# Kernel tuning notes

Hardware: AMD Instinct MI355X
Metric: run time of the kernel (lower is better)

The kernel has to match this reference:

```python
import jax, jax.numpy as jnp
import numpy as np

D_MODEL = 1024
D_STATE = 16
D_CONV = 4
EXPAND = 2
D_INNER = EXPAND * D_MODEL  # 2048
DT_RANK = 64  # ceil(1024/16)
BATCH = 2
SEQ = 1024
EPS = 1e-5


def _causal_depthwise_conv(x, w, b):
    # x: (B, L, D); w: (D, K) depthwise kernel; b: (D,)
    K = w.shape[1]
    xp = jnp.pad(x, ((0, 0), (K - 1, 0), (0, 0)))            # left-pad for causality
    out = jax.lax.conv_general_dilated(
        xp.transpose(0, 2, 1),          # (B, D, L+K-1)
        w[:, None, :],                  # (D, 1, K)
        window_strides=(1,), padding='VALID',
        feature_group_count=w.shape[0])
    return out.transpose(0, 2, 1) + b   # (B, L, D)


def _ssm_dir(xs, conv_w, conv_b, xproj_w, dt_w, dt_b, A_log, D_skip):
    # xs: (B, L, D_INNER)
    Bsz = xs.shape[0]
    xc = jax.nn.silu(_causal_depthwise_conv(xs, conv_w, conv_b))
    x_dbl = xc @ xproj_w                                        # (B, L, dt_rank + 2N)
    dt, B_ssm, C_ssm = jnp.split(x_dbl, [DT_RANK, DT_RANK + D_STATE], axis=-1)
    dt = jax.nn.softplus(dt @ dt_w + dt_b)                      # (B, L, D_INNER)
    A = -jnp.exp(A_log)                                         # (D_INNER, N)
    dA = jnp.exp(dt[..., None] * A)                             # (B, L, D_INNER, N)
    dBu = dt[..., None] * B_ssm[:, :, None, :] * xc[..., None]  # (B, L, D_INNER, N)

    def step(h, inp):
        dAt, dBut, ct = inp          # (B,D,N), (B,D,N), (B,N)
        h = dAt * h + dBut
        y = jnp.einsum('bdn,bn->bd', h, ct)
        return h, y

    h0 = jnp.zeros((Bsz, D_INNER, D_STATE), dtype=xs.dtype)
    _, ys = jax.lax.scan(step, h0,
                         (jnp.moveaxis(dA, 1, 0), jnp.moveaxis(dBu, 1, 0), jnp.moveaxis(C_ssm, 1, 0)))
    y = jnp.moveaxis(ys, 0, 1)                                  # (B, L, D_INNER)
    return y + xc * D_skip


def _layernorm(x, gamma, beta):
    mu = jnp.mean(x, axis=-1, keepdims=True)
    var = jnp.mean(jnp.square(x - mu), axis=-1, keepdims=True)
    return (x - mu) * jax.lax.rsqrt(var + EPS) * gamma + beta


def setup_inputs() -> dict:
    key = jax.random.key(0)
    ks = jax.random.split(key, 24)
    s = 0.02
    A_init = jnp.log(jnp.tile(jnp.arange(1, D_STATE + 1, dtype=jnp.float32)[None, :], (D_INNER, 1)))
    # dt bias init (inverse-softplus of small dt), as in the torch module
    dt0 = jnp.exp(jax.random.uniform(ks[20], (D_INNER,)) * (np.log(0.1) - np.log(0.001)) + np.log(0.001))
    dt0 = jnp.clip(dt0, 1e-4)
    inv_dt = dt0 + jnp.log(-jnp.expm1(-dt0))
    return {
        'x': jax.random.normal(ks[0], (BATCH, SEQ, D_MODEL), jnp.float32),
        'gamma': jnp.ones((D_MODEL,), jnp.float32),
        'beta': jnp.zeros((D_MODEL,), jnp.float32),
        'in_w': jax.random.normal(ks[1], (D_MODEL, 2 * D_INNER), jnp.float32) * s,
        'conv_w': jax.random.normal(ks[2], (D_INNER, D_CONV), jnp.float32) * s,
        'conv_b': jnp.zeros((D_INNER,), jnp.float32),
        'xproj_w': jax.random.normal(ks[3], (D_INNER, DT_RANK + 2 * D_STATE), jnp.float32) * s,
        'dt_w': jax.random.normal(ks[4], (DT_RANK, D_INNER), jnp.float32) * s,
        'dt_b': inv_dt,
        'A_log': A_init,
        'D_skip': jnp.ones((D_INNER,), jnp.float32),
        'conv_w_b': jax.random.normal(ks[5], (D_INNER, D_CONV), jnp.float32) * s,
        'conv_b_b': jnp.zeros((D_INNER,), jnp.float32),
        'xproj_w_b': jax.random.normal(ks[6], (D_INNER, DT_RANK + 2 * D_STATE), jnp.float32) * s,
        'dt_w_b': jax.random.normal(ks[7], (DT_RANK, D_INNER), jnp.float32) * s,
        'dt_b_b': inv_dt,
        'A_log_b': A_init,
        'D_skip_b': jnp.ones((D_INNER,), jnp.float32),
        'merge_w': jax.random.normal(ks[8], (2 * D_INNER, D_INNER), jnp.float32) * s,
        'out_w': jax.random.normal(ks[9], (D_INNER, D_MODEL), jnp.float32) * s,
    }


def reference(x, gamma, beta, in_w, conv_w, conv_b, xproj_w, dt_w, dt_b, A_log, D_skip,
              conv_w_b, conv_b_b, xproj_w_b, dt_w_b, dt_b_b, A_log_b, D_skip_b,
              merge_w, out_w):
    residual = x
    h = _layernorm(x, gamma, beta)
    xz = h @ in_w                               # (B, L, 2*D_INNER)
    xs, z = jnp.split(xz, 2, axis=-1)
    y_fwd = _ssm_dir(xs, conv_w, conv_b, xproj_w, dt_w, dt_b, A_log, D_skip)
    y_back = _ssm_dir(xs[:, ::-1], conv_w_b, conv_b_b, xproj_w_b, dt_w_b, dt_b_b, A_log_b, D_skip_b)[:, ::-1]
    y = jnp.concatenate([y_fwd, y_back], axis=-1) @ merge_w
    y = y * jax.nn.silu(z)
    y = y @ out_w
    return residual + y
```

## Files before the change

### kernel.cpp

```cpp
#include <hip/hip_runtime.h>
#include <hip/hip_bf16.h>
#include <math.h>

typedef __hip_bfloat16 bf16;
typedef unsigned int u32;
typedef __attribute__((ext_vector_type(8))) short bf16x8;
typedef __attribute__((ext_vector_type(4))) float f32x4;

#define BATCH 2
#define SEQ 1024
#define DM 1024
#define DI 2048
#define NST 16
#define DTR 64
#define XDN 96
#define XDP_LD 128
#define T_TOK 2048
#define N2 4096
#define NCHUNK 32
#define CLEN 32

static __device__ __forceinline__ float b2f(bf16 v) { return __bfloat162float(v); }
static __device__ __forceinline__ float bits2f(unsigned short u) {
    return __uint_as_float(((unsigned)u) << 16);
}

static __device__ __forceinline__ void gload_lds16(const void* g, void* l) {
    __builtin_amdgcn_global_load_lds((__attribute__((address_space(1))) u32*)(size_t)g,
                                     (__attribute__((address_space(3))) u32*)l, 16, 0, 0);
}

#define SBAR() do { asm volatile("" ::: "memory"); __builtin_amdgcn_s_barrier(); asm volatile("" ::: "memory"); } while (0)

static __device__ void tileT(const float* __restrict__ in, bf16* __restrict__ out,
                             int K, int N, int t, float (*tb)[33]) {
    int nt = N >> 5;
    int bx = (t % nt) << 5, by = (t / nt) << 5;
    int tx = threadIdx.x & 31, r0 = threadIdx.x >> 5;
#pragma unroll
    for (int r = r0; r < 32; r += 8)
        tb[r][tx] = in[(size_t)(by + r) * N + bx + tx];
    __syncthreads();
#pragma unroll
    for (int r = r0; r < 32; r += 8)
        out[(size_t)(bx + r) * K + by + tx] = __float2bfloat16(tb[tx][r]);
}

#define LN_BLKS   T_TOK
#define INW_T     ((N2 / 32) * (DM / 32))
#define OUTW_T    ((DM / 32) * (DI / 32))
#define MRGW_T    ((DI / 32) * (N2 / 32))
#define SMALL_BLK ((2 * XDP_LD * DI + 2 * DI * DTR) / 256)

__global__ __launch_bounds__(256) void prep_mega(const float* __restrict__ x,
                                                 const float* __restrict__ gamma,
                                                 const float* __restrict__ beta,
                                                 bf16* __restrict__ H,
                                                 const float* __restrict__ in_w, bf16* __restrict__ in_wT,
                                                 const float* __restrict__ out_w, bf16* __restrict__ out_wT,
                                                 const float* __restrict__ merge_w, bf16* __restrict__ merge_wT,
                                                 const float* __restrict__ xpf, const float* __restrict__ xpb,
                                                 bf16* __restrict__ XPF, bf16* __restrict__ XPB,
                                                 const float* __restrict__ dtwf, const float* __restrict__ dtwb,
                                                 bf16* __restrict__ dtwT) {
    __shared__ float tbuf[32][33];
    __shared__ float red[8];
    int bid = blockIdx.x;
    int tid = threadIdx.x;

    if (bid < LN_BLKS) {
        int t = bid;
        float xv[4];
        float s = 0.f, s2 = 0.f;
#pragma unroll
        for (int k = 0; k < 4; ++k) {
            float v = x[(size_t)t * DM + k * 256 + tid];
            xv[k] = v; s += v; s2 += v * v;
        }
#pragma unroll
        for (int off = 32; off; off >>= 1) {
            s  += __shfl_down(s, off);
            s2 += __shfl_down(s2, off);
        }
        int wid = tid >> 6, lane = tid & 63;
        if (!lane) { red[wid] = s; red[4 + wid] = s2; }
        __syncthreads();
        if (tid == 0) {
            float S = red[0] + red[1] + red[2] + red[3];
            float S2 = red[4] + red[5] + red[6] + red[7];
            float mu = S * (1.f / DM);
            float var = S2 * (1.f / DM) - mu * mu;
            red[0] = mu;
            red[1] = rsqrtf(var + 1e-5f);
        }
        __syncthreads();
        float mu = red[0], rs = red[1];
#pragma unroll
        for (int k = 0; k < 4; ++k) {
            int i = k * 256 + tid;
            H[(size_t)t * DM + i] = __float2bfloat16((xv[k] - mu) * rs * gamma[i] + beta[i]);
        }
        return;
    }
    bid -= LN_BLKS;
    if (bid < INW_T)  { tileT(in_w, in_wT, DM, N2, bid, tbuf); return; }
    bid -= INW_T;
    if (bid < OUTW_T) { tileT(out_w, out_wT, DI, DM, bid, tbuf); return; }
    bid -= OUTW_T;
    if (bid < MRGW_T) { tileT(merge_w, merge_wT, N2, DI, bid, tbuf); return; }
    bid -= MRGW_T;
    int idx = bid * 256 + tid;
    if (idx < 2 * XDP_LD * DI) {
        int dir = idx >= XDP_LD * DI;
        int i = idx - dir * (XDP_LD * DI);
        int n = i >> 11;
        int k = i & (DI - 1);
        float v = (n < XDN) ? (dir ? xpb : xpf)[k * XDN + n] : 0.f;
        (dir ? XPB : XPF)[i] = __float2bfloat16(v);
    } else {
        int j = idx - 2 * XDP_LD * DI;
        int dir = j >= DI * DTR;
        int e = j - dir * (DI * DTR);
        int n = e >> 6;
        int k = e & 63;
        dtwT[(size_t)dir * DI * DTR + n * DTR + k] =
            __float2bfloat16((dir ? dtwb : dtwf)[(size_t)k * DI + n]);
    }
}

template <int EPI>
__global__ __launch_bounds__(256) void mfma_gemm(const bf16* __restrict__ A,
                                                 const bf16* __restrict__ BT,
                                                 const bf16* __restrict__ BT2, int bysplit,
                                                 bf16* __restrict__ Cb,
                                                 const float* __restrict__ resid,
                                                 float* __restrict__ outf,
                                                 bf16* __restrict__ Pb,
                                                 const float* __restrict__ bias1,
                                                 const float* __restrict__ bias2,
                                                 int M, int N, int K) {
    __shared__ bf16 As[8192];
    __shared__ bf16 Bs[8192];
    int tid = threadIdx.x;
    int wave = tid >> 6, lane = tid & 63;
    int q = lane >> 4, ln16 = lane & 15;
    int bm = blockIdx.y * 128, bn = blockIdx.x * 128;
    int wm = (wave >> 1) * 64, wn = (wave & 1) * 64;
    const bf16* Bt = ((int)blockIdx.y < bysplit) ? BT : BT2;

    int ks = K / gridDim.z;
    int kb = blockIdx.z * ks;

    f32x4 zf; zf[0] = zf[1] = zf[2] = zf[3] = 0.f;
    f32x4 acc[4][4];
#pragma unroll
    for (int i = 0; i < 4; ++i)
#pragma unroll
        for (int j = 0; j < 4; ++j) acc[i][j] = zf;

    for (int k0 = kb; k0 < kb + ks; k0 += 64) {
#pragma unroll
        for (int i = 0; i < 4; ++i) {
            int s = wave * 256 + i * 64 + lane;
            int kg = s >> 7, m = s & 127;
            gload_lds16(&A[(size_t)(bm + m) * K + k0 + kg * 8], &As[(wave * 256 + i * 64) * 8]);
            gload_lds16(&Bt[(size_t)(bn + m) * K + k0 + kg * 8], &Bs[(wave * 256 + i * 64) * 8]);
        }
        __syncthreads();
#pragma unroll
        for (int kk = 0; kk < 2; ++kk) {
            bf16x8 af[4], bfr[4];
#pragma unroll
            for (int i = 0; i < 4; ++i) {
                af[i]  = *(const bf16x8*)&As[(((kk * 4 + q) * 128) + (wm + i * 16 + ln16)) * 8];
                bfr[i] = *(const bf16x8*)&Bs[(((kk * 4 + q) * 128) + (wn + i * 16 + ln16)) * 8];
            }
#pragma unroll
            for (int i = 0; i < 4; ++i)
#pragma unroll
                for (int j = 0; j < 4; ++j)
                    acc[i][j] = __builtin_amdgcn_mfma_f32_16x16x32_bf16(af[i], bfr[j], acc[i][j], 0, 0, 0);
        }
        __syncthreads();
    }

    size_t pbase = (size_t)blockIdx.z * M * N;
#pragma unroll
    for (int i = 0; i < 4; ++i)
#pragma unroll
        for (int r = 0; r < 4; ++r) {
            int row = bm + wm + i * 16 + q * 4 + r;
            const float* bias = (EPI == 4) ? ((row < T_TOK) ? bias1 : bias2) : nullptr;
#pragma unroll
            for (int j = 0; j < 4; ++j) {
                int col = bn + wn + j * 16 + ln16;
                size_t idx = (size_t)row * N + col;
                float v = acc[i][j][r];
                if (EPI == 0)      Cb[idx] = __float2bfloat16(v);
                else if (EPI == 1) outf[idx] = resid[idx] + v;
                else if (EPI == 2) outf[idx] = v;
                else if (EPI == 3) Pb[pbase + idx] = __float2bfloat16(v);
                else {
                    float t = v + bias[col];
                    float sp = (t > 20.f) ? t : log1pf(__expf(t));
                    Cb[idx] = __float2bfloat16(sp);
                }
            }
        }
}

template <int EPI>
__global__ __launch_bounds__(512, 2) void gemm256(const bf16* __restrict__ A,
                                                  const bf16* __restrict__ BT,
                                                  bf16* __restrict__ Cb,
                                                  bf16* __restrict__ Pb,
                                                  int M, int N, int K) {
    __shared__ bf16 LA[4][8192];
    __shared__ bf16 LB[4][8192];
    int tid = threadIdx.x;
    int wave = tid >> 6, lane = tid & 63;
    int q = lane >> 4, ln16 = lane & 15;
    int bm = blockIdx.y * 256, bn = blockIdx.x * 256;
    int wm = (wave >> 2) * 128, wn = (wave & 3) * 64;
    int ksz = K / gridDim.z;
    int kb = blockIdx.z * ksz;
    int NT = ksz >> 5;

    int o0 = tid * 16, o1 = 8192 + tid * 16;
    int r0 = o0 >> 6, r1 = o1 >> 6;
    int c0 = (o0 & 63) ^ (((r0 >> 1) & 3) << 4);
    int c1 = (o1 & 63) ^ (((r1 >> 1) & 3) << 4);
    const bf16* pa0 = &A[(size_t)(bm + r0) * K + kb + (c0 >> 1)];
    const bf16* pa1 = &A[(size_t)(bm + r1) * K + kb + (c1 >> 1)];
    const bf16* pb0 = &BT[(size_t)(bn + r0) * K + kb + (c0 >> 1)];
    const bf16* pb1 = &BT[(size_t)(bn + r1) * K + kb + (c1 >> 1)];
    int d0 = wave * 512;
    int d1 = 4096 + wave * 512;

    int aoff[8], boff[4];
#pragma unroll
    for (int i = 0; i < 8; ++i) {
        int r = wm + i * 16 + ln16;
        aoff[i] = (r * 64 + q * 16) ^ (((r >> 1) & 3) << 4);
    }
#pragma unroll
    for (int j = 0; j < 4; ++j) {
        int r = wn + j * 16 + ln16;
        boff[j] = (r * 64 + q * 16) ^ (((r >> 1) & 3) << 4);
    }

    f32x4 zf; zf[0] = zf[1] = zf[2] = zf[3] = 0.f;
    f32x4 acc[8][4];
#pragma unroll
    for (int i = 0; i < 8; ++i)
#pragma unroll
        for (int j = 0; j < 4; ++j) acc[i][j] = zf;

    auto STAGE = [&](int b, int koff) {
        gload_lds16(pa0 + koff, &LA[b][d0]);
        gload_lds16(pa1 + koff, &LA[b][d1]);
        gload_lds16(pb0 + koff, &LB[b][d0]);
        gload_lds16(pb1 + koff, &LB[b][d1]);
    };

#define RD_FRAGS(AV, BV, TT) do {                                             \
        const bf16* LAb_ = LA[(TT) & 3];                                      \
        const bf16* LBb_ = LB[(TT) & 3];                                      \
        _Pragma("unroll")                                                     \
        for (int j_ = 0; j_ < 4; ++j_) BV[j_] = *(const bf16x8*)&LBb_[boff[j_] >> 1]; \
        _Pragma("unroll")                                                     \
        for (int i_ = 0; i_ < 8; ++i_) AV[i_] = *(const bf16x8*)&LAb_[aoff[i_] >> 1]; \
    } while (0)

#define MFMA_ALL(AV, BV) do {                                                 \
        __builtin_amdgcn_s_setprio(1);                                        \
        _Pragma("unroll")                                                     \
        for (int i_ = 0; i_ < 8; ++i_)                                        \
            _Pragma("unroll")                                                 \
            for (int j_ = 0; j_ < 4; ++j_)                                    \
                acc[i_][j_] = __builtin_amdgcn_mfma_f32_16x16x32_bf16(AV[i_], BV[j_], acc[i_][j_], 0, 0, 0); \
        __builtin_amdgcn_s_setprio(0);                                        \
    } while (0)

    bf16x8 avX[8], bvX[4], avY[8], bvY[4];

    STAGE(0, 0); STAGE(1, 32); STAGE(2, 64);
    asm volatile("s_waitcnt vmcnt(4)" ::: "memory");
    SBAR();
    RD_FRAGS(avX, bvX, 0);

    for (int t = 0; t < NT; t += 2) {
        if (t + 1 < NT) RD_FRAGS(avY, bvY, t + 1);
        if (t + 3 < NT) STAGE((t + 3) & 3, (t + 3) * 32);
        MFMA_ALL(avX, bvX);
        if (t + 3 < NT)      asm volatile("s_waitcnt vmcnt(4)" ::: "memory");
        else if (t + 2 < NT) asm volatile("s_waitcnt vmcnt(0)" ::: "memory");
        SBAR();
        if (t + 2 < NT) RD_FRAGS(avX, bvX, t + 2);
        if (t + 4 < NT) STAGE((t + 4) & 3, (t + 4) * 32);
        MFMA_ALL(avY, bvY);
        if (t + 4 < NT)      asm volatile("s_waitcnt vmcnt(4)" ::: "memory");
        else if (t + 3 < NT) asm volatile("s_waitcnt vmcnt(0)" ::: "memory");
        SBAR();
    }
#undef RD_FRAGS
#undef MFMA_ALL

    size_t pbase = (size_t)blockIdx.z * ((size_t)M * N);
#pragma unroll
    for (int i = 0; i < 8; ++i)
#pragma unroll
        for (int r = 0; r < 4; ++r) {
            int row = bm + wm + i * 16 + q * 4 + r;
#pragma unroll
            for (int j = 0; j < 4; ++j) {
                int col = bn + wn + j * 16 + ln16;
                size_t idx = (size_t)row * N + col;
                float v = acc[i][j][r];
                if (EPI == 0) Cb[idx] = __float2bfloat16(v);
                else          Pb[pbase + idx] = __float2bfloat16(v);
            }
        }
}

__global__ __launch_bounds__(256) void reduce_plain(const bf16* __restrict__ P, int ns, size_t MN,
                                                    bf16* __restrict__ O) {
    size_t i = ((size_t)blockIdx.x * 256 + threadIdx.x) * 4;
    float s[4] = {0.f, 0.f, 0.f, 0.f};
    for (int k = 0; k < ns; ++k) {
        ushort4 p = *reinterpret_cast<const ushort4*>(&P[(size_t)k * MN + i]);
        s[0] += bits2f(p.x); s[1] += bits2f(p.y); s[2] += bits2f(p.z); s[3] += bits2f(p.w);
    }
    bf16 r[4];
#pragma unroll
    for (int j = 0; j < 4; ++j) r[j] = __float2bfloat16(s[j]);
    *reinterpret_cast<ushort4*>(&O[i]) = *reinterpret_cast<ushort4*>(r);
}

__global__ __launch_bounds__(256) void reduce_gate(const bf16* __restrict__ P, int ns, size_t MN,
                                                   const bf16* __restrict__ XZ, bf16* __restrict__ YM) {
    size_t i = ((size_t)blockIdx.x * 256 + threadIdx.x) * 4;
    float s[4] = {0.f, 0.f, 0.f, 0.f};
    for (int k = 0; k < ns; ++k) {
        ushort4 p = *reinterpret_cast<const ushort4*>(&P[(size_t)k * MN + i]);
        s[0] += bits2f(p.x); s[1] += bits2f(p.y); s[2] += bits2f(p.z); s[3] += bits2f(p.w);
    }
    int t = (int)(i >> 11), c = (int)(i & (DI - 1));
    const bf16* zp = &XZ[(size_t)t * N2 + DI + c];
    bf16 r[4];
#pragma unroll
    for (int j = 0; j < 4; ++j) {
        float z = b2f(zp[j]);
        r[j] = __float2bfloat16(s[j] * (z / (1.f + __expf(-z))));
    }
    *reinterpret_cast<ushort4*>(&YM[i]) = *reinterpret_cast<ushort4*>(r);
}

__global__ __launch_bounds__(256) void reduce_out(const bf16* __restrict__ P, int ns, size_t MN,
                                                  const float* __restrict__ x, float* __restrict__ out) {
    size_t i = ((size_t)blockIdx.x * 256 + threadIdx.x) * 4;
    float s[4] = {0.f, 0.f, 0.f, 0.f};
    for (int k = 0; k < ns; ++k) {
        ushort4 p = *reinterpret_cast<const ushort4*>(&P[(size_t)k * MN + i]);
        s[0] += bits2f(p.x); s[1] += bits2f(p.y); s[2] += bits2f(p.z); s[3] += bits2f(p.w);
    }
    float4 xv = *reinterpret_cast<const float4*>(&x[i]);
    float4 o = {s[0] + xv.x, s[1] + xv.y, s[2] + xv.z, s[3] + xv.w};
    *reinterpret_cast<float4*>(&out[i]) = o;
}

__global__ __launch_bounds__(256) void reduce_xdbl(const bf16* __restrict__ P, int ns, size_t MN,
                                                   float* __restrict__ XDP, bf16* __restrict__ XDdt) {
    size_t i = ((size_t)blockIdx.x * 256 + threadIdx.x) * 4;
    float s[4] = {0.f, 0.f, 0.f, 0.f};
    for (int k = 0; k < ns; ++k) {
        ushort4 p = *reinterpret_cast<const ushort4*>(&P[(size_t)k * MN + i]);
        s[0] += bits2f(p.x); s[1] += bits2f(p.y); s[2] += bits2f(p.z); s[3] += bits2f(p.w);
    }
    float4 o = {s[0], s[1], s[2], s[3]};
    *reinterpret_cast<float4*>(&XDP[i]) = o;
    int col = (int)(i & (XDP_LD - 1));
    if (col < DTR) {
        size_t row = i >> 7;
        bf16 r[4];
#pragma unroll
        for (int j = 0; j < 4; ++j) r[j] = __float2bfloat16(s[j]);
        *reinterpret_cast<ushort4*>(&XDdt[row * DTR + col]) = *reinterpret_cast<ushort4*>(r);
    }
}

__global__ __launch_bounds__(256) void gemm_dt(const float* __restrict__ A,
                                               const float* __restrict__ Bw,
                                               const float* __restrict__ bias,
                                               bf16* __restrict__ Cb, int M, int N) {
    __shared__ float As[16][68];
    __shared__ float Bs[16][68];
    int tid = threadIdx.x;
    int bm = blockIdx.y * 64, bn = blockIdx.x * 64;
    int tx = tid & 15, ty = tid >> 4;
    float acc[4][4];
#pragma unroll
    for (int i = 0; i < 4; ++i)
#pragma unroll
        for (int j = 0; j < 4; ++j) acc[i][j] = 0.f;
    int arow = tid >> 2, acg = (tid & 3) * 4;
    int brow = tid >> 4, bcol = (tid & 15) * 4;
    for (int k0 = 0; k0 < DTR; k0 += 16) {
        float4 av = *reinterpret_cast<const float4*>(&A[(size_t)(bm + arow) * XDP_LD + k0 + acg]);
        As[acg + 0][arow] = av.x; As[acg + 1][arow] = av.y;
        As[acg + 2][arow] = av.z; As[acg + 3][arow] = av.w;
        float4 bv = *reinterpret_cast<const float4*>(&Bw[(size_t)(k0 + brow) * N + bn + bcol]);
        Bs[brow][bcol + 0] = bv.x; Bs[brow][bcol + 1] = bv.y;
        Bs[brow][bcol + 2] = bv.z; Bs[brow][bcol + 3] = bv.w;
        __syncthreads();
#pragma unroll
        for (int kk = 0; kk < 16; ++kk) {
            float4 a = *reinterpret_cast<const float4*>(&As[kk][ty * 4]);
            float4 b = *reinterpret_cast<const float4*>(&Bs[kk][tx * 4]);
            acc[0][0] += a.x * b.x; acc[0][1] += a.x * b.y; acc[0][2] += a.x * b.z; acc[0][3] += a.x * b.w;
            acc[1][0] += a.y * b.x; acc[1][1] += a.y * b.y; acc[1][2] += a.y * b.z; acc[1][3] += a.y * b.w;
            acc[2][0] += a.z * b.x; acc[2][1] += a.z * b.y; acc[2][2] += a.z * b.z; acc[2][3] += a.z * b.w;
            acc[3][0] += a.w * b.x; acc[3][1] += a.w * b.y; acc[3][2] += a.w * b.z; acc[3][3] += a.w * b.w;
        }
        __syncthreads();
    }
    int row0 = bm + ty * 4, col0 = bn + tx * 4;
#pragma unroll
    for (int i = 0; i < 4; ++i)
#pragma unroll
        for (int j = 0; j < 4; ++j) {
            float v = acc[i][j] + bias[col0 + j];
            float sp = (v > 20.f) ? v : log1pf(__expf(v));
            Cb[(size_t)(row0 + i) * N + col0 + j] = __float2bfloat16(sp);
        }
}

__global__ __launch_bounds__(256) void conv_kernel(const bf16* __restrict__ XZ,
                                                   const float* __restrict__ wf, const float* __restrict__ bf_,
                                                   const float* __restrict__ wb, const float* __restrict__ bb_,
                                                   bf16* __restrict__ XCF, bf16* __restrict__ XCB) {
    int idx = blockIdx.x * 256 + threadIdx.x;
    int c = idx & (DI - 1);
    int g = idx >> 11;
    int l = g & (SEQ - 1);
    int b = g >> 10;
    float sf = bf_[c];
    float sb = bb_[c];
#pragma unroll
    for (int j = 0; j < 4; ++j) {
        int lf = l - 3 + j;
        if (lf >= 0) sf += wf[c * 4 + j] * b2f(XZ[((size_t)(b * SEQ + lf)) * N2 + c]);
        int lb = l + 3 - j;
        if (lb < SEQ) sb += wb[c * 4 + j] * b2f(XZ[((size_t)(b * SEQ + lb)) * N2 + c]);
    }
    XCF[idx] = __float2bfloat16(sf / (1.f + __expf(-sf)));
    XCB[idx] = __float2bfloat16(sb / (1.f + __expf(-sb)));
}

template <bool FINAL>
__global__ __launch_bounds__(256) void scan_chunk(const bf16* __restrict__ DTF_, const bf16* __restrict__ DTB_,
                                                  const bf16* __restrict__ XCF_, const bf16* __restrict__ XCB_,
                                                  const float* __restrict__ XDP,
                                                  const float* __restrict__ Af, const float* __restrict__ Ab,
                                                  const float* __restrict__ Df, const float* __restrict__ Db,
                                                  float* __restrict__ HLOC, float* __restrict__ SUMDT,
                                                  bf16* __restrict__ YCAT) {
    __shared__ float bsl[CLEN][32];
    int c = blockIdx.x * 256 + threadIdx.x;
    int b = blockIdx.y;
    int dir = blockIdx.z >> 5, chunk = blockIdx.z & 31;
    {
        int it = threadIdx.x >> 3, j4 = (threadIdx.x & 7) * 4;
        int sit = chunk * CLEN + it;
        int l = dir ? (SEQ - 1 - sit) : sit;
        size_t row = (size_t)dir * T_TOK + (size_t)b * SEQ + l;
        *(float4*)&bsl[it][j4] = *(const float4*)&XDP[row * XDP_LD + DTR + j4];
    }
    const bf16* DT = dir ? DTB_ : DTF_;
    const bf16* XC = dir ? XCB_ : XCF_;
    const float* Al = dir ? Ab : Af;
    float A[NST];
#pragma unroll
    for (int n = 0; n < NST; ++n) A[n] = -__expf(Al[c * NST + n]);
    size_t base = ((((size_t)dir * BATCH + b) * NCHUNK + chunk) * DI + c);
    float h[NST];
    float Dv = 0.f;
    if (FINAL) {
#pragma unroll
        for (int n = 0; n < NST; ++n) h[n] = HLOC[base * NST + n];
        Dv = (dir ? Db : Df)[c];
    } else {
#pragma unroll
        for (int n = 0; n < NST; ++n) h[n] = 0.f;
    }
    __syncthreads();
    float sumdt = 0.f;
    for (int it = 0; it < CLEN; ++it) {
        int sit = chunk * CLEN + it;
        int l = dir ? (SEQ - 1 - sit) : sit;
        size_t g = (size_t)b * SEQ + l;
        float dt = b2f(DT[g * DI + c]);
        float xc = b2f(XC[g * DI + c]);
        float dtxc = dt * xc;
        const float* bs = bsl[it];
        if (FINAL) {
            float y = 0.f;
#pragma unroll
            for (int n = 0; n < NST; ++n) {
                h[n] = __expf(dt * A[n]) * h[n] + dtxc * bs[n];
                y += h[n] * bs[NST + n];
            }
            YCAT[g * N2 + dir * DI + c] = __float2bfloat16(y + xc * Dv);
        } else {
            sumdt += dt;
#pragma unroll
            for (int n = 0; n < NST; ++n)
                h[n] = __expf(dt * A[n]) * h[n] + dtxc * bs[n];
        }
    }
    if (!FINAL) {
#pragma unroll
        for (int n = 0; n < NST; ++n) HLOC[base * NST + n] = h[n];
        SUMDT[base] = sumdt;
    }
}

__global__ __launch_bounds__(256) void scan_combine(float* __restrict__ HLOC,
                                                    const float* __restrict__ SUMDT,
                                                    const float* __restrict__ Af,
                                                    const float* __restrict__ Ab) {
    int idx = blockIdx.x * 256 + threadIdx.x;
    int n = idx & 15;
    int c = (idx >> 4) & (DI - 1);
    int b = (idx >> 15) & 1;
    int dir = idx >> 16;
    float A = -__expf((dir ? Ab : Af)[c * NST + n]);
    float h = 0.f;
    for (int k = 0; k < NCHUNK; ++k) {
        size_t base = ((((size_t)dir * BATCH + b) * NCHUNK + k) * DI + c);
        float P = __expf(A * SUMDT[base]);
        float hl = HLOC[base * NST + n];
        HLOC[base * NST + n] = h;
        h = P * h + hl;
    }
}

__global__ __launch_bounds__(256) void gate_kernel(bf16* __restrict__ YM, const bf16* __restrict__ XZ) {
    int idx = blockIdx.x * 256 + threadIdx.x;
    int t = idx >> 11;
    int c = idx & (DI - 1);
    float z = b2f(XZ[(size_t)t * N2 + DI + c]);
    float y = b2f(YM[idx]);
    YM[idx] = __float2bfloat16(y * (z / (1.f + __expf(-z))));
}

extern "C" void kernel_launch(void* const* d_in, const int* in_sizes, int n_in,
                              void* d_out, int out_size, void* d_ws, size_t ws_size,
                              hipStream_t stream) {
    const float* x       = (const float*)d_in[0];
    const float* gamma   = (const float*)d_in[1];
    const float* beta    = (const float*)d_in[2];
    const float* in_w    = (const float*)d_in[3];
    const float* conv_w  = (const float*)d_in[4];
    const float* conv_b  = (const float*)d_in[5];
    const float* xproj_w = (const float*)d_in[6];
    const float* dt_w    = (const float*)d_in[7];
    const float* dt_b    = (const float*)d_in[8];
    const float* A_log   = (const float*)d_in[9];
    const float* D_skip  = (const float*)d_in[10];
    const float* conv_w_b  = (const float*)d_in[11];
    const float* conv_b_b  = (const float*)d_in[12];
    const float* xproj_w_b = (const float*)d_in[13];
    const float* dt_w_b    = (const float*)d_in[14];
    const float* dt_b_b    = (const float*)d_in[15];
    const float* A_log_b   = (const float*)d_in[16];
    const float* D_skip_b  = (const float*)d_in[17];
    const float* merge_w   = (const float*)d_in[18];
    const float* out_w     = (const float*)d_in[19];
    float* out = (float*)d_out;

    char* w = (char*)d_ws;
    size_t off = 0;
    bf16* H       = (bf16*)(w + off); off += (size_t)T_TOK * DM * 2;
    bf16* XZ      = (bf16*)(w + off); off += (size_t)T_TOK * N2 * 2;
    bf16* XCF     = (bf16*)(w + off); off += (size_t)T_TOK * DI * 2;
    bf16* XCB     = (bf16*)(w + off); off += (size_t)T_TOK * DI * 2;
    bf16* XPF     = (bf16*)(w + off); off += (size_t)XDP_LD * DI * 2;
    bf16* XPB     = (bf16*)(w + off); off += (size_t)XDP_LD * DI * 2;
    float* XDP    = (float*)(w + off); off += (size_t)2 * T_TOK * XDP_LD * 4;
    bf16* DTF     = (bf16*)(w + off); off += (size_t)T_TOK * DI * 2;
    bf16* DTB     = (bf16*)(w + off); off += (size_t)T_TOK * DI * 2;
    bf16* YCAT    = (bf16*)(w + off); off += (size_t)T_TOK * N2 * 2;
    bf16* in_wT   = (bf16*)(w + off); off += (size_t)N2 * DM * 2;
    bf16* out_wT  = (bf16*)(w + off); off += (size_t)DM * DI * 2;
    bf16* merge_wT= (bf16*)(w + off); off += (size_t)DI * N2 * 2;
    bf16* dtwT    = (bf16*)(w + off); off += (size_t)2 * DI * DTR * 2;
    bf16* XDdt    = (bf16*)(w + off); off += (size_t)2 * T_TOK * DTR * 2;
    char* PART = w + off;
    size_t avail = (ws_size > off) ? ws_size - off : 0;

    float* HLOC  = (float*)PART;
    float* SUMDT = (float*)(PART + (size_t)2 * BATCH * NCHUNK * DI * NST * 4);
    bf16* Pb     = (bf16*)PART;
    bf16* YM     = DTF;

    size_t MNm = (size_t)T_TOK * DI;
    size_t MNo = (size_t)T_TOK * DM;
    size_t MNx = (size_t)2 * T_TOK * XDP_LD;
    size_t MNz = (size_t)T_TOK * N2;
    int s_merge = (avail >= 4 * MNm * 2) ? 4 : (avail >= 2 * MNm * 2) ? 2 : 0;
    int s_out   = (avail >= 4 * MNo * 2) ? 4 : (avail >= 2 * MNo * 2) ? 2 : 0;
    int s_xdbl  = (avail >= 16 * MNx * 2) ? 16 : (avail >= 8 * MNx * 2) ? 8 : (avail >= 4 * MNx * 2) ? 4 : 0;
    int s_xz    = (avail >= 2 * MNz * 2) ? 2 : 0;

    prep_mega<<<LN_BLKS + INW_T + OUTW_T + MRGW_T + SMALL_BLK, 256, 0, stream>>>(
        x, gamma, beta, H, in_w, in_wT, out_w, out_wT, merge_w, merge_wT,
        xproj_w, xproj_w_b, XPF, XPB, dt_w, dt_w_b, dtwT);
    if (s_xz) {
        gemm256<3><<<dim3(N2 / 256, T_TOK / 256, s_xz), 512, 0, stream>>>(
            H, in_wT, nullptr, Pb, T_TOK, N2, DM);
        reduce_plain<<<(int)(MNz / 4 / 256), 256, 0, stream>>>(Pb, s_xz, MNz, XZ);
    } else {
        mfma_gemm<0><<<dim3(N2 / 128, T_TOK / 128), 256, 0, stream>>>(
            H, in_wT, in_wT, 1 << 30, XZ, nullptr, nullptr, nullptr, nullptr, nullptr, T_TOK, N2, DM);
    }
    conv_kernel<<<(T_TOK * DI) / 256, 256, 0, stream>>>(XZ, conv_w, conv_b, conv_w_b, conv_b_b, XCF, XCB);
    if (s_xdbl) {
        mfma_gemm<3><<<dim3(1, (2 * T_TOK) / 128, s_xdbl), 256, 0, stream>>>(
            XCF, XPF, XPB, (T_TOK / 128), nullptr, nullptr, nullptr, Pb, nullptr, nullptr,
            2 * T_TOK, XDP_LD, DI);
        reduce_xdbl<<<(int)(MNx / 4 / 256), 256, 0, stream>>>(Pb, s_xdbl, MNx, XDP, XDdt);
        mfma_gemm<4><<<dim3(DI / 128, (2 * T_TOK) / 128), 256, 0, stream>>>(
            XDdt, dtwT, dtwT + (size_t)DI * DTR, (T_TOK / 128), DTF, nullptr, nullptr, nullptr,
            dt_b, dt_b_b, 2 * T_TOK, DI, DTR);
    } else {
        mfma_gemm<2><<<dim3(1, (2 * T_TOK) / 128), 256, 0, stream>>>(
            XCF, XPF, XPB, (T_TOK / 128), nullptr, nullptr, XDP, nullptr, nullptr, nullptr,
            2 * T_TOK, XDP_LD, DI);
        gemm_dt<<<dim3(DI / 64, T_TOK / 64), 256, 0, stream>>>(XDP, dt_w, dt_b, DTF, T_TOK, DI);
        gemm_dt<<<dim3(DI / 64, T_TOK / 64), 256, 0, stream>>>(XDP + (size_t)T_TOK * XDP_LD, dt_w_b, dt_b_b, DTB, T_TOK, DI);
    }
    scan_chunk<false><<<dim3(DI / 256, BATCH, 2 * NCHUNK), 256, 0, stream>>>(
        DTF, DTB, XCF, XCB, XDP, A_log, A_log_b, D_skip, D_skip_b, HLOC, SUMDT, YCAT);
    scan_combine<<<(2 * BATCH * DI * NST) / 256, 256, 0, stream>>>(HLOC, SUMDT, A_log, A_log_b);
    scan_chunk<true><<<dim3(DI / 256, BATCH, 2 * NCHUNK), 256, 0, stream>>>(
        DTF, DTB, XCF, XCB, XDP, A_log, A_log_b, D_skip, D_skip_b, HLOC, SUMDT, YCAT);
    if (s_merge) {
        gemm256<3><<<dim3(DI / 256, T_TOK / 256, s_merge), 512, 0, stream>>>(
            YCAT, merge_wT, nullptr, Pb, T_TOK, DI, N2);
        reduce_gate<<<(int)(MNm / 4 / 256), 256, 0, stream>>>(Pb, s_merge, MNm, XZ, YM);
    } else {
        mfma_gemm<0><<<dim3(DI / 128, T_TOK / 128), 256, 0, stream>>>(
            YCAT, merge_wT, merge_wT, 1 << 30, YM, nullptr, nullptr, nullptr, nullptr, nullptr,
            T_TOK, DI, N2);
        gate_kernel<<<(T_TOK * DI) / 256, 256, 0, stream>>>(YM, XZ);
    }
    if (s_out) {
        mfma_gemm<3><<<dim3(DM / 128, T_TOK / 128, s_out), 256, 0, stream>>>(
            YM, out_wT, out_wT, 1 << 30, nullptr, nullptr, nullptr, Pb, nullptr, nullptr,
            T_TOK, DM, DI);
        reduce_out<<<(int)(MNo / 4 / 256), 256, 0, stream>>>(Pb, s_out, MNo, x, out);
    } else {
        mfma_gemm<1><<<dim3(DM / 128, T_TOK / 128), 256, 0, stream>>>(
            YM, out_wT, out_wT, 1 << 30, nullptr, x, out, nullptr, nullptr, nullptr,
            T_TOK, DM, DI);
    }
}
```

Before: 433.2 us.

## Restructure GEMM main loop into eight-phase ping-pong with interleaved loads and barriers

Replaces the three-stage-ahead prefetch loop of the 256x256 GEMM with a two-K-tile-per-iteration schedule. Each K tile is split into four MFMA quadrants, with LDS fragment reads, single global-to-LDS loads and block barriers interleaved between them, similar to HipKittens-style 8-wave ping-pong. The goal is to spread memory traffic across the MFMA stream and keep fewer fragment registers live. In exchange it adds many more barriers per tile, and its correctness assumes the per-block K tile count is even.

```diff
diff --git a/kernel.cpp b/kernel.cpp
--- a/kernel.cpp
+++ b/kernel.cpp
@@ -224,7 +224,8 @@
     int wm = (wave >> 2) * 128, wn = (wave & 3) * 64;
     int ksz = K / gridDim.z;
     int kb = blockIdx.z * ksz;
-    int NT = ksz >> 5;
+    int NPG = ksz >> 5;
+    int NIT = NPG >> 1;
 
     int o0 = tid * 16, o1 = 8192 + tid * 16;
     int r0 = o0 >> 6, r1 = o1 >> 6;
@@ -256,55 +257,96 @@
 #pragma unroll
         for (int j = 0; j < 4; ++j) acc[i][j] = zf;
 
-    auto STAGE = [&](int b, int koff) {
-        gload_lds16(pa0 + koff, &LA[b][d0]);
-        gload_lds16(pa1 + koff, &LA[b][d1]);
-        gload_lds16(pb0 + koff, &LB[b][d0]);
-        gload_lds16(pb1 + koff, &LB[b][d1]);
-    };
-
-#define RD_FRAGS(AV, BV, TT) do {                                             \
-        const bf16* LAb_ = LA[(TT) & 3];                                      \
-        const bf16* LBb_ = LB[(TT) & 3];                                      \
-        _Pragma("unroll")                                                     \
-        for (int j_ = 0; j_ < 4; ++j_) BV[j_] = *(const bf16x8*)&LBb_[boff[j_] >> 1]; \
-        _Pragma("unroll")                                                     \
-        for (int i_ = 0; i_ < 8; ++i_) AV[i_] = *(const bf16x8*)&LAb_[aoff[i_] >> 1]; \
-    } while (0)
-
-#define MFMA_ALL(AV, BV) do {                                                 \
-        __builtin_amdgcn_s_setprio(1);                                        \
-        _Pragma("unroll")                                                     \
-        for (int i_ = 0; i_ < 8; ++i_)                                        \
-            _Pragma("unroll")                                                 \
-            for (int j_ = 0; j_ < 4; ++j_)                                    \
-                acc[i_][j_] = __builtin_amdgcn_mfma_f32_16x16x32_bf16(AV[i_], BV[j_], acc[i_][j_], 0, 0, 0); \
-        __builtin_amdgcn_s_setprio(0);                                        \
-    } while (0)
-
-    bf16x8 avX[8], bvX[4], avY[8], bvY[4];
-
-    STAGE(0, 0); STAGE(1, 32); STAGE(2, 64);
+    gload_lds16(pa0,      &LA[0][d0]); gload_lds16(pa1,      &LA[0][d1]);
+    gload_lds16(pb0,      &LB[0][d0]); gload_lds16(pb1,      &LB[0][d1]);
+    gload_lds16(pa0 + 32, &LA[1][d0]); gload_lds16(pa1 + 32, &LA[1][d1]);
+    gload_lds16(pb0 + 32, &LB[1][d0]); gload_lds16(pb1 + 32, &LB[1][d1]);
     asm volatile("s_waitcnt vmcnt(4)" ::: "memory");
     SBAR();
-    RD_FRAGS(avX, bvX, 0);
-
-    for (int t = 0; t < NT; t += 2) {
-        if (t + 1 < NT) RD_FRAGS(avY, bvY, t + 1);
-        if (t + 3 < NT) STAGE((t + 3) & 3, (t + 3) * 32);
-        MFMA_ALL(avX, bvX);
-        if (t + 3 < NT)      asm volatile("s_waitcnt vmcnt(4)" ::: "memory");
-        else if (t + 2 < NT) asm volatile("s_waitcnt vmcnt(0)" ::: "memory");
-        SBAR();
-        if (t + 2 < NT) RD_FRAGS(avX, bvX, t + 2);
-        if (t + 4 < NT) STAGE((t + 4) & 3, (t + 4) * 32);
-        MFMA_ALL(avY, bvY);
-        if (t + 4 < NT)      asm volatile("s_waitcnt vmcnt(4)" ::: "memory");
-        else if (t + 3 < NT) asm volatile("s_waitcnt vmcnt(0)" ::: "memory");
-        SBAR();
-    }
-#undef RD_FRAGS
-#undef MFMA_ALL
+
+    bf16x8 aL[4], aH[4], bL[2], bH[2];
+
+#define MQ(I0, J0, AV, BV)                                                     \
+    _Pragma("unroll")                                                          \
+    for (int ii_ = 0; ii_ < 4; ++ii_)                                          \
+        _Pragma("unroll")                                                      \
+        for (int jj_ = 0; jj_ < 2; ++jj_)                                      \
+            acc[(I0) + ii_][(J0) + jj_] = __builtin_amdgcn_mfma_f32_16x16x32_bf16( \
+                AV[ii_], BV[jj_], acc[(I0) + ii_][(J0) + jj_], 0, 0, 0)
+
+    for (int i = 0; i < NIT; ++i) {
+        int p0 = (2 * i) & 3, p1 = p0 + 1;
+        int s0 = p0 ^ 2, s1 = s0 + 1;
+        int kA = (2 * i + 2) * 32, kB = (2 * i + 3) * 32;
+        bool st = (i + 1 < NIT);
+        const bf16* A0 = LA[p0]; const bf16* B0 = LB[p0];
+        const bf16* A1 = LA[p1]; const bf16* B1 = LB[p1];
+
+#pragma unroll
+        for (int u = 0; u < 4; ++u) aL[u] = *(const bf16x8*)&A0[aoff[u] >> 1];
+#pragma unroll
+        for (int u = 0; u < 2; ++u) bL[u] = *(const bf16x8*)&B0[boff[u] >> 1];
+        if (st) gload_lds16(pa0 + kA, &LA[s0][d0]);
+        SBAR();
+        __builtin_amdgcn_s_setprio(1); MQ(0, 0, aL, bL); __builtin_amdgcn_s_setprio(0);
+        SBAR();
+
+#pragma unroll
+        for (int u = 0; u < 2; ++u) bH[u] = *(const bf16x8*)&B0[boff[2 + u] >> 1];
+        if (st) gload_lds16(pa1 + kA, &LA[s0][d1]);
+        SBAR();
+        __builtin_amdgcn_s_setprio(1); MQ(0, 2, aL, bH); __builtin_amdgcn_s_setprio(0);
+        SBAR();
+
+#pragma unroll
+        for (int u = 0; u < 4; ++u) aH[u] = *(const bf16x8*)&A0[aoff[4 + u] >> 1];
+        if (st) gload_lds16(pb0 + kA, &LB[s0][d0]);
+        SBAR();
+        __builtin_amdgcn_s_setprio(1); MQ(4, 0, aH, bL); __builtin_amdgcn_s_setprio(0);
+        SBAR();
+
+        if (st) {
+            gload_lds16(pb1 + kA, &LB[s0][d1]);
+            asm volatile("s_waitcnt vmcnt(4)" ::: "memory");
+        } else {
+            asm volatile("s_waitcnt vmcnt(0)" ::: "memory");
+        }
+        SBAR();
+        __builtin_amdgcn_s_setprio(1); MQ(4, 2, aH, bH); __builtin_amdgcn_s_setprio(0);
+        SBAR();
+
+#pragma unroll
+        for (int u = 0; u < 4; ++u) aL[u] = *(const bf16x8*)&A1[aoff[u] >> 1];
+#pragma unroll
+        for (int u = 0; u < 2; ++u) bL[u] = *(const bf16x8*)&B1[boff[u] >> 1];
+        if (st) gload_lds16(pa0 + kB, &LA[s1][d0]);
+        SBAR();
+        __builtin_amdgcn_s_setprio(1); MQ(0, 0, aL, bL); __builtin_amdgcn_s_setprio(0);
+        SBAR();
+
+#pragma unroll
+        for (int u = 0; u < 2; ++u) bH[u] = *(const bf16x8*)&B1[boff[2 + u] >> 1];
+        if (st) gload_lds16(pa1 + kB, &LA[s1][d1]);
+        SBAR();
+        __builtin_amdgcn_s_setprio(1); MQ(0, 2, aL, bH); __builtin_amdgcn_s_setprio(0);
+        SBAR();
+
+#pragma unroll
+        for (int u = 0; u < 4; ++u) aH[u] = *(const bf16x8*)&A1[aoff[4 + u] >> 1];
+        if (st) gload_lds16(pb0 + kB, &LB[s1][d0]);
+        SBAR();
+        __builtin_amdgcn_s_setprio(1); MQ(4, 0, aH, bL); __builtin_amdgcn_s_setprio(0);
+        SBAR();
+
+        if (st) {
+            gload_lds16(pb1 + kB, &LB[s1][d1]);
+            asm volatile("s_waitcnt vmcnt(4)" ::: "memory");
+        }
+        SBAR();
+        __builtin_amdgcn_s_setprio(1); MQ(4, 2, aH, bH); __builtin_amdgcn_s_setprio(0);
+        SBAR();
+    }
+#undef MQ
 
     size_t pbase = (size_t)blockIdx.z * ((size_t)M * N);
 #pragma unroll
```

After: 444.9 us. 1.03x slower.
